# Performance work log

Measured on AMD Instinct MI355X. Metric: run time of the kernel, lower is better.

## Reference

```python
import jax, jax.numpy as jnp
import numpy as np

B, NQ, ISIZE = 8, 2048, 1024
H, D, NA = 8, 128, 8            # num_head, attn_dim, num_anchor
AH = H * D                      # ahsize = 1024
ASZ = NA * D                    # anchor_size = 1024
FH = 4096                       # _fhsize
ISZ_NET = FH * H // NA          # 4096, input dim of self.net
EPS = 1e-6


def setup_inputs() -> dict:
    key = jax.random.key(0)
    ks = jax.random.split(key, 12)
    def u(k, shape, fan_in):
        s = 1.0 / np.sqrt(fan_in)
        return jax.random.uniform(k, shape, jnp.float32, -s, s)
    return {
        "inputs": jax.random.normal(ks[0], (B, NQ, ISIZE), jnp.float32),
        "ln_g": jnp.ones((ISIZE,), jnp.float32),
        "ln_b": jnp.zeros((ISIZE,), jnp.float32),
        "q_anchor": u(ks[1], (H, NA, D), D),
        "W_qkv": u(ks[2], (ISIZE, 3 * AH), ISIZE), "b_qkv": jnp.zeros((3 * AH,), jnp.float32),
        "W_an": u(ks[3], (ASZ, FH), ASZ), "b_an": jnp.zeros((FH,), jnp.float32),
        "W_n1": u(ks[4], (ISZ_NET, AH), ISZ_NET), "b_n1": jnp.zeros((AH,), jnp.float32),
        "W_n2": u(ks[5], (AH, FH), AH), "b_n2": jnp.zeros((FH,), jnp.float32),
        "W_n3": u(ks[6], (FH, AH), FH), "b_n3": jnp.zeros((AH,), jnp.float32),
        "W_k": u(ks[7], (AH, AH), AH), "b_k": jnp.zeros((AH,), jnp.float32),
        "W_o": u(ks[8], (AH, ISIZE), AH), "b_o": jnp.zeros((ISIZE,), jnp.float32),
    }


def reference(inputs, ln_g, ln_b, q_anchor, W_qkv, b_qkv, W_an, b_an,
              W_n1, b_n1, W_n2, b_n2, W_n3, b_n3, W_k, b_k, W_o, b_o):
    b, nq = inputs.shape[:2]
    scale = 1.0 / np.sqrt(D)
    # pre-LayerNorm
    mu = jnp.mean(inputs, -1, keepdims=True)
    var = jnp.mean(jnp.square(inputs - mu), -1, keepdims=True)
    x = (inputs - mu) * jax.lax.rsqrt(var + EPS) * ln_g + ln_b
    # QKV projection
    qkv = (x @ W_qkv + b_qkv).reshape(b, nq, 3, H, D)
    q = jnp.transpose(qkv[:, :, 0], (0, 2, 1, 3))   # [b,H,nq,D]
    k = qkv[:, :, 1]                                  # [b,nq,H,D]
    v = qkv[:, :, 2]                                  # [b,nq,H,D]
    # stage 1: fixed anchors attend over the sequence
    sc1 = jax.nn.softmax(jnp.einsum('had,bnhd->bhan', q_anchor, k) * scale, axis=-1)
    out = jnp.einsum('bhan,bnhd->bhad', sc1, v).reshape(b, H, ASZ)   # [b,H,NA*D]
    # anchor_net (share_head Linear + ReLU)
    out = jax.nn.relu(out @ W_an + b_an)                              # [b,H,FH]
    # regroup head-major -> anchor-major
    out = out.reshape(b, H, NA, FH // NA).transpose(0, 2, 1, 3).reshape(b, NA, ISZ_NET)
    # net: bottleneck Linear -> Linear -> ReLU -> Linear
    out = jax.nn.relu((out @ W_n1 + b_n1) @ W_n2 + b_n2) @ W_n3 + b_n3  # [b,NA,AH]
    # stage 2: queries attend over anchors
    kk = (out @ W_k + b_k).reshape(b, NA, H, D)
    sc2 = jax.nn.softmax(jnp.einsum('bhqd,bahd->bhqa', q, kk) * scale, axis=-1)
    ov = out.reshape(b, NA, H, D)
    y = jnp.einsum('bhqa,bahd->bqhd', sc2, ov).reshape(b, nq, AH)
    return y @ W_o + b_o + inputs
```

## Files before the change

### kernel.cpp

```cpp
#include <hip/hip_runtime.h>
#include <cstdint>
#include <cstddef>

typedef unsigned short u16;
typedef __attribute__((ext_vector_type(8))) short short8;
typedef __attribute__((ext_vector_type(4))) float floatx4;

__device__ __forceinline__ u16 f2bf(float f) {
  unsigned u = __float_as_uint(f);
  u += 0x7fffu + ((u >> 16) & 1u);
  return (u16)(u >> 16);
}
__device__ __forceinline__ float bf2f(u16 s) {
  return __uint_as_float(((unsigned)s) << 16);
}

__global__ __launch_bounds__(256) void ln_kernel(const float* __restrict__ x,
                                                 const float* __restrict__ g,
                                                 const float* __restrict__ bta,
                                                 u16* __restrict__ out) {
  const int row = blockIdx.x;
  const int tid = threadIdx.x;
  const float4 v = ((const float4*)(x + (size_t)row * 1024))[tid];
  float s = v.x + v.y + v.z + v.w;
#pragma unroll
  for (int o = 32; o > 0; o >>= 1) s += __shfl_down(s, o);
  __shared__ float red[4], red2[4];
  const int wv = tid >> 6, ln = tid & 63;
  if (ln == 0) red[wv] = s;
  __syncthreads();
  const float mean = (red[0] + red[1] + red[2] + red[3]) * (1.0f / 1024.0f);
  const float dx = v.x - mean, dy = v.y - mean, dz = v.z - mean, dw = v.w - mean;
  float s2 = dx * dx + dy * dy + dz * dz + dw * dw;
#pragma unroll
  for (int o = 32; o > 0; o >>= 1) s2 += __shfl_down(s2, o);
  if (ln == 0) red2[wv] = s2;
  __syncthreads();
  const float var = (red2[0] + red2[1] + red2[2] + red2[3]) * (1.0f / 1024.0f);
  const float rstd = rsqrtf(var + 1e-6f);
  const float4 gg = ((const float4*)g)[tid];
  const float4 bb = ((const float4*)bta)[tid];
  ushort4 o4;
  o4.x = f2bf(dx * rstd * gg.x + bb.x);
  o4.y = f2bf(dy * rstd * gg.y + bb.y);
  o4.z = f2bf(dz * rstd * gg.z + bb.z);
  o4.w = f2bf(dw * rstd * gg.w + bb.w);
  ((ushort4*)(out + (size_t)row * 1024))[tid] = o4;
}

__global__ __launch_bounds__(256) void transpose_bf16(const float* __restrict__ W,
                                                      u16* __restrict__ WT,
                                                      int K, int N) {
  __shared__ float t[32][33];
  const int kb = blockIdx.x * 32, nb = blockIdx.y * 32;
  const int tx = threadIdx.x & 31, ty = threadIdx.x >> 5;
#pragma unroll
  for (int i = ty; i < 32; i += 8) t[i][tx] = W[(size_t)(kb + i) * N + nb + tx];
  __syncthreads();
#pragma unroll
  for (int i = ty; i < 32; i += 8) WT[(size_t)(nb + i) * K + kb + tx] = f2bf(t[tx][i]);
}


__device__ __forceinline__ void stage2(const u16* __restrict__ src, u16* dst,
                                       int growbase, int kcol, int ld,
                                       int wave, int lane) {
#pragma unroll
  for (int i = 0; i < 2; ++i) {
    const int row = (i * 8 + wave) * 8 + (lane >> 3);
    const u16* gp = src + (size_t)(growbase + row) * ld + kcol + (((lane & 7) ^ (row & 7)) << 3);
    u16* lp = dst + (i * 8 + wave) * 512;
    __builtin_amdgcn_global_load_lds((const __attribute__((address_space(1))) void*)gp,
                                     (__attribute__((address_space(3))) void*)lp, 16, 0, 0);
  }
}

__device__ __forceinline__ void rdA4(short8 (&af)[4][2], const u16* sbuf, int half,
                                     int wr, int fr, int fq) {
#pragma unroll
  for (int mi = 0; mi < 4; ++mi)
#pragma unroll
    for (int ks = 0; ks < 2; ++ks) {
      const int row = half * 128 + wr * 64 + mi * 16 + fr;
      const int kg = ks * 4 + fq;
      af[mi][ks] = *(const short8*)(sbuf + row * 64 + ((kg ^ (row & 7)) << 3));
    }
}

__device__ __forceinline__ void rdB2(short8 (&bfr)[2][2], const u16* sbuf, int half,
                                     int wc, int fr, int fq) {
#pragma unroll
  for (int ni = 0; ni < 2; ++ni)
#pragma unroll
    for (int ks = 0; ks < 2; ++ks) {
      const int row = half * 128 + wc * 32 + ni * 16 + fr;
      const int kg = ks * 4 + fq;
      bfr[ni][ks] = *(const short8*)(sbuf + row * 64 + ((kg ^ (row & 7)) << 3));
    }
}

template <int Q>
__device__ __forceinline__ void mfmaQ(floatx4 (&acc)[4][4][2], const short8 (&af)[4][2],
                                      const short8 (&bfr)[2][2]) {
#pragma unroll
  for (int mi = 0; mi < 4; ++mi)
#pragma unroll
    for (int ni = 0; ni < 2; ++ni)
      acc[Q][mi][ni] = __builtin_amdgcn_mfma_f32_16x16x32_bf16(af[mi][0], bfr[ni][0], acc[Q][mi][ni], 0, 0, 0);
#pragma unroll
  for (int mi = 0; mi < 4; ++mi)
#pragma unroll
    for (int ni = 0; ni < 2; ++ni)
      acc[Q][mi][ni] = __builtin_amdgcn_mfma_f32_16x16x32_bf16(af[mi][1], bfr[ni][1], acc[Q][mi][ni], 0, 0, 0);
}

template <int B_>
__device__ __forceinline__ void gtile(int t, int NT, int K,
                                      u16 (&sA)[2][16384], u16 (&sB)[2][16384],
                                      const u16* __restrict__ A, const u16* __restrict__ BT,
                                      int m0, int n0, int wave, int lane,
                                      int wr, int wc, int fr, int fq,
                                      floatx4 (&acc)[4][4][2]) {
  short8 af[4][2], bfr[2][2];
  rdA4(af, sA[B_], 0, wr, fr, fq);
  rdB2(bfr, sB[B_], 0, wc, fr, fq);
  if (t + 1 < NT) stage2(A, &sA[B_ ^ 1][8192], m0 + 128, (t + 1) << 6, K, wave, lane);
  asm volatile("s_waitcnt lgkmcnt(0)" ::: "memory");
  __builtin_amdgcn_sched_barrier(0);
  __builtin_amdgcn_s_setprio(1);
  mfmaQ<0>(acc, af, bfr);
  __builtin_amdgcn_s_setprio(0);
  rdB2(bfr, sB[B_], 1, wc, fr, fq);
  if (t + 1 < NT) stage2(BT, &sB[B_ ^ 1][0], n0, (t + 1) << 6, K, wave, lane);
  asm volatile("s_waitcnt lgkmcnt(0)" ::: "memory");
  __builtin_amdgcn_sched_barrier(0);
  __builtin_amdgcn_s_setprio(1);
  mfmaQ<1>(acc, af, bfr);
  __builtin_amdgcn_s_setprio(0);
  rdA4(af, sA[B_], 1, wr, fr, fq);
  __builtin_amdgcn_s_barrier();
  if (t + 2 < NT) stage2(A, &sA[B_][0], m0, (t + 2) << 6, K, wave, lane);
  asm volatile("s_waitcnt lgkmcnt(0)" ::: "memory");
  __builtin_amdgcn_sched_barrier(0);
  __builtin_amdgcn_s_setprio(1);
  mfmaQ<2>(acc, af, bfr);
  __builtin_amdgcn_s_setprio(0);
  rdB2(bfr, sB[B_], 0, wc, fr, fq);
  if (t + 2 < NT) stage2(BT, &sB[B_][8192], n0 + 128, (t + 2) << 6, K, wave, lane);
  asm volatile("s_waitcnt lgkmcnt(0)" ::: "memory");
  __builtin_amdgcn_sched_barrier(0);
  __builtin_amdgcn_s_setprio(1);
  mfmaQ<3>(acc, af, bfr);
  __builtin_amdgcn_s_setprio(0);
  if (t + 2 < NT) {
    asm volatile("s_waitcnt vmcnt(4)" ::: "memory");
  } else {
    asm volatile("s_waitcnt vmcnt(0)" ::: "memory");
  }
  __builtin_amdgcn_s_barrier();
}

template <int EPI>
__global__ __launch_bounds__(512, 2) void gemm_bf16(const u16* __restrict__ A,
                                                    const u16* __restrict__ BT,
                                                    const float* __restrict__ bias,
                                                    const float* __restrict__ extra,
                                                    u16* __restrict__ outB,
                                                    float* __restrict__ outF,
                                                    int M, int N, int K) {
  __shared__ u16 sA[2][16384];
  __shared__ u16 sB[2][16384];
  const int tid = threadIdx.x;
  const int wave = tid >> 6, lane = tid & 63;
  const int m0 = blockIdx.x * 256, n0 = blockIdx.y * 256;
  const int wr = wave >> 2, wc = wave & 3;
  const int fr = lane & 15, fq = lane >> 4;
  const int NT = K >> 6;

  floatx4 acc[4][4][2];
  const floatx4 zero = {0.f, 0.f, 0.f, 0.f};
#pragma unroll
  for (int q = 0; q < 4; ++q)
#pragma unroll
    for (int i = 0; i < 4; ++i)
#pragma unroll
      for (int j = 0; j < 2; ++j) acc[q][i][j] = zero;

  stage2(A, &sA[0][0], m0, 0, K, wave, lane);
  stage2(A, &sA[0][8192], m0 + 128, 0, K, wave, lane);
  stage2(BT, &sB[0][0], n0, 0, K, wave, lane);
  stage2(BT, &sB[0][8192], n0 + 128, 0, K, wave, lane);
  stage2(A, &sA[1][0], m0, 64, K, wave, lane);
  stage2(BT, &sB[1][8192], n0 + 128, 64, K, wave, lane);
  asm volatile("s_waitcnt vmcnt(4)" ::: "memory");
  __builtin_amdgcn_s_barrier();

  for (int t = 0; t < NT; t += 2) {
    gtile<0>(t, NT, K, sA, sB, A, BT, m0, n0, wave, lane, wr, wc, fr, fq, acc);
    gtile<1>(t + 1, NT, K, sA, sB, A, BT, m0, n0, wave, lane, wr, wc, fr, fq, acc);
  }

#pragma unroll
  for (int q = 0; q < 4; ++q) {
    const int QM = q >> 1, QN = QM ^ (q & 1);
#pragma unroll
    for (int mi = 0; mi < 4; ++mi)
#pragma unroll
      for (int ni = 0; ni < 2; ++ni)
#pragma unroll
        for (int r = 0; r < 4; ++r) {
          const int m = m0 + QM * 128 + wr * 64 + mi * 16 + fq * 4 + r;
          const int n = n0 + QN * 128 + wc * 32 + ni * 16 + fr;
          const float v = acc[q][mi][ni][r] + bias[n];
          if (EPI == 0)
            outB[(size_t)m * N + n] = f2bf(v);
          else
            outF[(size_t)m * N + n] = v + extra[(size_t)m * N + n];
        }
  }
}

__global__ __launch_bounds__(256) void attn1_scores(const u16* __restrict__ qkv,
                                                    const float* __restrict__ q_anchor,
                                                    float* __restrict__ S) {
  __shared__ float qa[8][128];
  const int tid = threadIdx.x;
  const int chunk = blockIdx.x & 7, bh = blockIdx.x >> 3;
  const int b = bh >> 3, h = bh & 7;
  for (int i = tid; i < 1024; i += 256) qa[i >> 7][i & 127] = q_anchor[h * 1024 + i];
  __syncthreads();
  const float scale = 0.0883883476483184f;
  const int n = chunk * 256 + tid;
  const u16* kp = qkv + (size_t)(b * 2048 + n) * 3072 + 1024 + h * 128;
  float dots[8] = {0, 0, 0, 0, 0, 0, 0, 0};
#pragma unroll 8
  for (int dd = 0; dd < 128; dd += 4) {
    const ushort4 k4 = *(const ushort4*)(kp + dd);
    const float k0 = bf2f(k4.x), k1 = bf2f(k4.y), k2 = bf2f(k4.z), k3 = bf2f(k4.w);
#pragma unroll
    for (int a = 0; a < 8; ++a) {
      const float4 q4 = *(const float4*)&qa[a][dd];
      dots[a] += q4.x * k0 + q4.y * k1 + q4.z * k2 + q4.w * k3;
    }
  }
#pragma unroll
  for (int a = 0; a < 8; ++a) S[((size_t)(bh * 8 + a)) * 2048 + n] = dots[a] * scale;
}

__global__ __launch_bounds__(256) void attn1_softmax(float* __restrict__ S) {
  const int row = blockIdx.x;
  const int tid = threadIdx.x;
  float* Sp = S + (size_t)row * 2048;
  float4 v0 = ((const float4*)Sp)[tid * 2];
  float4 v1 = ((const float4*)Sp)[tid * 2 + 1];
  float mx = fmaxf(fmaxf(fmaxf(v0.x, v0.y), fmaxf(v0.z, v0.w)),
                   fmaxf(fmaxf(v1.x, v1.y), fmaxf(v1.z, v1.w)));
#pragma unroll
  for (int o = 32; o > 0; o >>= 1) mx = fmaxf(mx, __shfl_xor(mx, o));
  __shared__ float red[4];
  const int wv = tid >> 6, ln = tid & 63;
  if (ln == 0) red[wv] = mx;
  __syncthreads();
  mx = fmaxf(fmaxf(red[0], red[1]), fmaxf(red[2], red[3]));
  v0.x = __expf(v0.x - mx); v0.y = __expf(v0.y - mx);
  v0.z = __expf(v0.z - mx); v0.w = __expf(v0.w - mx);
  v1.x = __expf(v1.x - mx); v1.y = __expf(v1.y - mx);
  v1.z = __expf(v1.z - mx); v1.w = __expf(v1.w - mx);
  float sum = v0.x + v0.y + v0.z + v0.w + v1.x + v1.y + v1.z + v1.w;
#pragma unroll
  for (int o = 32; o > 0; o >>= 1) sum += __shfl_xor(sum, o);
  __shared__ float red2[4];
  if (ln == 0) red2[wv] = sum;
  __syncthreads();
  const float inv = 1.f / (red2[0] + red2[1] + red2[2] + red2[3]);
  v0.x *= inv; v0.y *= inv; v0.z *= inv; v0.w *= inv;
  v1.x *= inv; v1.y *= inv; v1.z *= inv; v1.w *= inv;
  ((float4*)Sp)[tid * 2] = v0;
  ((float4*)Sp)[tid * 2 + 1] = v1;
}

__global__ __launch_bounds__(256) void attn1_pv(const u16* __restrict__ qkv,
                                                const float* __restrict__ S,
                                                float* __restrict__ pvpart) {
  __shared__ float P[8][256];
  const int tid = threadIdx.x;
  const int chunk = blockIdx.x & 7, bh = blockIdx.x >> 3;
  const int b = bh >> 3, h = bh & 7;
  for (int i = tid; i < 2048; i += 256) {
    const int a = i >> 8, n = i & 255;
    P[a][n] = S[((size_t)(bh * 8 + a)) * 2048 + chunk * 256 + n];
  }
  __syncthreads();
  const int d = tid & 127, half = tid >> 7;
  const int nbase = chunk * 256 + half * 128;
  const u16* vp = qkv + (size_t)(b * 2048 + nbase) * 3072 + 2048 + h * 128 + d;
  float acc[8] = {0.f};
  for (int n = 0; n < 128; n += 4) {
    const float v0 = bf2f(vp[(size_t)n * 3072]);
    const float v1 = bf2f(vp[(size_t)(n + 1) * 3072]);
    const float v2 = bf2f(vp[(size_t)(n + 2) * 3072]);
    const float v3 = bf2f(vp[(size_t)(n + 3) * 3072]);
#pragma unroll
    for (int a = 0; a < 8; ++a) {
      const float4 s4 = *(const float4*)&P[a][half * 128 + n];
      acc[a] += s4.x * v0 + s4.y * v1 + s4.z * v2 + s4.w * v3;
    }
  }
  const int split = chunk * 2 + half;
#pragma unroll
  for (int a = 0; a < 8; ++a)
    pvpart[((size_t)split * 64 + bh) * 1024 + a * 128 + d] = acc[a];
}

__global__ __launch_bounds__(256) void mlp_mfma(const float* __restrict__ A,
                                                const float* __restrict__ W,
                                                float* __restrict__ part,
                                                int K, int N, int KC) {
  __shared__ float sW[64][33];
  const int tid = threadIdx.x;
  const int lane = tid & 63, wave = tid >> 6;
  const int wm = wave * 16;
  const int n0 = blockIdx.x * 64;
  const int kbeg = blockIdx.y * KC;
  const int l15 = lane & 15, kq8 = (lane >> 4) * 8;
  const int arow = wm + l15;

  floatx4 acc[4];
  const floatx4 zero = {0.f, 0.f, 0.f, 0.f};
#pragma unroll
  for (int j = 0; j < 4; ++j) acc[j] = zero;

  for (int kc = 0; kc < KC; kc += 32) {
    const int kbase = kbeg + kc;
    __syncthreads();
#pragma unroll
    for (int p = 0; p < 8; ++p) {
      const int k = p * 4 + wave;
      sW[lane][k] = W[(size_t)(kbase + k) * N + n0 + lane];
    }
    const float* ap = A + (size_t)arow * K + kbase + kq8;
    const float4 a0 = *(const float4*)ap;
    const float4 a1 = *(const float4*)(ap + 4);
    short8 af;
    af[0] = (short)f2bf(a0.x); af[1] = (short)f2bf(a0.y);
    af[2] = (short)f2bf(a0.z); af[3] = (short)f2bf(a0.w);
    af[4] = (short)f2bf(a1.x); af[5] = (short)f2bf(a1.y);
    af[6] = (short)f2bf(a1.z); af[7] = (short)f2bf(a1.w);
    __syncthreads();
#pragma unroll
    for (int j = 0; j < 4; ++j) {
      const float* wp = &sW[j * 16 + l15][kq8];
      short8 bf;
      bf[0] = (short)f2bf(wp[0]); bf[1] = (short)f2bf(wp[1]);
      bf[2] = (short)f2bf(wp[2]); bf[3] = (short)f2bf(wp[3]);
      bf[4] = (short)f2bf(wp[4]); bf[5] = (short)f2bf(wp[5]);
      bf[6] = (short)f2bf(wp[6]); bf[7] = (short)f2bf(wp[7]);
      acc[j] = __builtin_amdgcn_mfma_f32_16x16x32_bf16(af, bf, acc[j], 0, 0, 0);
    }
  }
  const int q = lane >> 4;
#pragma unroll
  for (int j = 0; j < 4; ++j)
#pragma unroll
    for (int r = 0; r < 4; ++r) {
      const int m = wm + q * 4 + r;
      const int n = n0 + j * 16 + l15;
      part[((size_t)blockIdx.y * 64 + m) * N + n] = acc[j][r];
    }
}

__global__ __launch_bounds__(256) void mlp_reduce(const float* __restrict__ part,
                                                  const float* __restrict__ bias,
                                                  float* __restrict__ out,
                                                  int N, int nsplit, int relu, int perm) {
  const int idx = blockIdx.x * 256 + threadIdx.x;
  const int e = idx * 4;
  if (e >= 64 * N) return;
  const int row = e / N, col = e - row * N;
  float4 acc;
  if (bias) acc = *(const float4*)&bias[col];
  else { acc.x = 0.f; acc.y = 0.f; acc.z = 0.f; acc.w = 0.f; }
  for (int s = 0; s < nsplit; ++s) {
    const float4 p = *(const float4*)&part[((size_t)s * 64 + row) * N + col];
    acc.x += p.x; acc.y += p.y; acc.z += p.z; acc.w += p.w;
  }
  if (relu) {
    acc.x = fmaxf(acc.x, 0.f); acc.y = fmaxf(acc.y, 0.f);
    acc.z = fmaxf(acc.z, 0.f); acc.w = fmaxf(acc.w, 0.f);
  }
  size_t oidx;
  if (!perm) {
    oidx = (size_t)row * N + col;
  } else {
    const int b = row >> 3, h = row & 7;
    oidx = (size_t)(b * 8 + (col >> 9)) * 4096 + h * 512 + (col & 511);
  }
  *(float4*)&out[oidx] = acc;
}

__global__ __launch_bounds__(256) void attn2_kernel(const u16* __restrict__ qkv,
                                                    const float* __restrict__ kk,
                                                    const float* __restrict__ onet,
                                                    u16* __restrict__ y) {
  __shared__ float kkl[8][128];
  __shared__ float ovl[8][128];
  const int tid = threadIdx.x;
  const int chunk = blockIdx.x & 7, bh = blockIdx.x >> 3;
  const int b = bh >> 3, h = bh & 7;
  for (int i = tid; i < 1024; i += 256) {
    const int a = i >> 7, d = i & 127;
    kkl[a][d] = kk[(size_t)(b * 8 + a) * 1024 + h * 128 + d];
    ovl[a][d] = onet[(size_t)(b * 8 + a) * 1024 + h * 128 + d];
  }
  __syncthreads();
  const int n = chunk * 256 + tid;
  const u16* qp = qkv + (size_t)(b * 2048 + n) * 3072 + h * 128;
  float dots[8] = {0, 0, 0, 0, 0, 0, 0, 0};
#pragma unroll 4
  for (int dd = 0; dd < 128; dd += 4) {
    const ushort4 q4 = *(const ushort4*)(qp + dd);
    const float q0 = bf2f(q4.x), q1 = bf2f(q4.y), q2 = bf2f(q4.z), q3 = bf2f(q4.w);
#pragma unroll
    for (int a = 0; a < 8; ++a) {
      const float4 k4 = *(const float4*)&kkl[a][dd];
      dots[a] += k4.x * q0 + k4.y * q1 + k4.z * q2 + k4.w * q3;
    }
  }
  const float scale = 0.0883883476483184f;
  float mx = -1e30f;
#pragma unroll
  for (int a = 0; a < 8; ++a) {
    dots[a] *= scale;
    mx = fmaxf(mx, dots[a]);
  }
  float p[8];
  float sum = 0.f;
#pragma unroll
  for (int a = 0; a < 8; ++a) {
    p[a] = __expf(dots[a] - mx);
    sum += p[a];
  }
  const float inv = 1.f / sum;
#pragma unroll
  for (int a = 0; a < 8; ++a) p[a] *= inv;
  u16* yp = y + (size_t)(b * 2048 + n) * 1024 + h * 128;
#pragma unroll 4
  for (int dd = 0; dd < 128; dd += 4) {
    float a0 = 0, a1 = 0, a2 = 0, a3 = 0;
#pragma unroll
    for (int a = 0; a < 8; ++a) {
      const float4 o4 = *(const float4*)&ovl[a][dd];
      a0 += p[a] * o4.x;
      a1 += p[a] * o4.y;
      a2 += p[a] * o4.z;
      a3 += p[a] * o4.w;
    }
    ushort4 o;
    o.x = f2bf(a0);
    o.y = f2bf(a1);
    o.z = f2bf(a2);
    o.w = f2bf(a3);
    *(ushort4*)(yp + dd) = o;
  }
}

extern "C" void kernel_launch(void* const* d_in, const int* in_sizes, int n_in,
                              void* d_out, int out_size, void* d_ws, size_t ws_size,
                              hipStream_t stream) {
  const float* inputs = (const float*)d_in[0];
  const float* ln_g = (const float*)d_in[1];
  const float* ln_b = (const float*)d_in[2];
  const float* q_anchor = (const float*)d_in[3];
  const float* W_qkv = (const float*)d_in[4];
  const float* b_qkv = (const float*)d_in[5];
  const float* W_an = (const float*)d_in[6];
  const float* b_an = (const float*)d_in[7];
  const float* W_n1 = (const float*)d_in[8];
  const float* b_n1 = (const float*)d_in[9];
  const float* W_n2 = (const float*)d_in[10];
  const float* b_n2 = (const float*)d_in[11];
  const float* W_n3 = (const float*)d_in[12];
  const float* b_n3 = (const float*)d_in[13];
  const float* W_k = (const float*)d_in[14];
  const float* b_k = (const float*)d_in[15];
  const float* W_o = (const float*)d_in[16];
  const float* b_o = (const float*)d_in[17];
  float* out = (float*)d_out;

  char* ws = (char*)d_ws;
  u16* qkv = (u16*)(ws);
  u16* xbf = (u16*)(ws + 100663296);
  float* S = (float*)(ws + 100663296);
  float* part = (float*)(ws + 109051904);
  u16* WqkvT = (u16*)(ws + 134217728);
  u16* WoT = (u16*)(ws + 140509184);
  float* att1 = (float*)(ws + 142606336);
  float* anp = (float*)(ws + 142868480);
  float* h1 = (float*)(ws + 143917056);
  float* h2 = (float*)(ws + 144179200);
  float* onet = (float*)(ws + 145227776);
  float* kkb = (float*)(ws + 145489920);

  ln_kernel<<<16384, 256, 0, stream>>>(inputs, ln_g, ln_b, xbf);
  transpose_bf16<<<dim3(32, 96), 256, 0, stream>>>(W_qkv, WqkvT, 1024, 3072);
  transpose_bf16<<<dim3(32, 32), 256, 0, stream>>>(W_o, WoT, 1024, 1024);
  gemm_bf16<0><<<dim3(64, 12), 512, 0, stream>>>(xbf, WqkvT, b_qkv, nullptr, qkv, nullptr,
                                                 16384, 3072, 1024);
  attn1_scores<<<512, 256, 0, stream>>>(qkv, q_anchor, S);
  attn1_softmax<<<512, 256, 0, stream>>>(S);
  attn1_pv<<<512, 256, 0, stream>>>(qkv, S, part);
  mlp_reduce<<<64, 256, 0, stream>>>(part, nullptr, att1, 1024, 16, 0, 0);
  mlp_mfma<<<dim3(64, 8), 256, 0, stream>>>(att1, W_an, part, 1024, 4096, 128);
  mlp_reduce<<<256, 256, 0, stream>>>(part, b_an, anp, 4096, 8, 1, 1);
  mlp_mfma<<<dim3(16, 32), 256, 0, stream>>>(anp, W_n1, part, 4096, 1024, 128);
  mlp_reduce<<<64, 256, 0, stream>>>(part, b_n1, h1, 1024, 32, 0, 0);
  mlp_mfma<<<dim3(64, 8), 256, 0, stream>>>(h1, W_n2, part, 1024, 4096, 128);
  mlp_reduce<<<256, 256, 0, stream>>>(part, b_n2, h2, 4096, 8, 1, 0);
  mlp_mfma<<<dim3(16, 32), 256, 0, stream>>>(h2, W_n3, part, 4096, 1024, 128);
  mlp_reduce<<<64, 256, 0, stream>>>(part, b_n3, onet, 1024, 32, 0, 0);
  mlp_mfma<<<dim3(16, 16), 256, 0, stream>>>(onet, W_k, part, 1024, 1024, 64);
  mlp_reduce<<<64, 256, 0, stream>>>(part, b_k, kkb, 1024, 16, 0, 0);
  attn2_kernel<<<512, 256, 0, stream>>>(qkv, kkb, onet, xbf);
  gemm_bf16<1><<<dim3(64, 4), 512, 0, stream>>>(xbf, WoT, b_o, inputs, nullptr, out,
                                                16384, 1024, 1024);
}
```

Before: 586.4 us.

## Switch GEMM to 32x32x16 MFMA with precomputed LDS offsets and reordered staging

Replaces the 16x16x32 bf16 MFMA tiling in the main GEMM with 32x32x16 instructions (2x1 fragments per quarter, 4 k-steps). LDS read offsets and global staging pointers are precomputed once per thread instead of recomputed each tile, and the quarter schedule reuses B fragments across quarters with a partial lgkmcnt wait. The intent is to cut LDS read traffic and issue overhead per FLOP. It also reshapes the epilogue to the 32x32 output layout, which keeps scattered per-element stores.

```diff
diff --git a/kernel.cpp b/kernel.cpp
--- a/kernel.cpp
+++ b/kernel.cpp
@@ -5,6 +5,7 @@
 typedef unsigned short u16;
 typedef __attribute__((ext_vector_type(8))) short short8;
 typedef __attribute__((ext_vector_type(4))) float floatx4;
+typedef __attribute__((ext_vector_type(16))) float floatx16;
 
 __device__ __forceinline__ u16 f2bf(float f) {
   unsigned u = __float_as_uint(f);
@@ -62,95 +63,75 @@
 }
 
 
-__device__ __forceinline__ void stage2(const u16* __restrict__ src, u16* dst,
-                                       int growbase, int kcol, int ld,
-                                       int wave, int lane) {
-#pragma unroll
-  for (int i = 0; i < 2; ++i) {
-    const int row = (i * 8 + wave) * 8 + (lane >> 3);
-    const u16* gp = src + (size_t)(growbase + row) * ld + kcol + (((lane & 7) ^ (row & 7)) << 3);
-    u16* lp = dst + (i * 8 + wave) * 512;
-    __builtin_amdgcn_global_load_lds((const __attribute__((address_space(1))) void*)gp,
-                                     (__attribute__((address_space(3))) void*)lp, 16, 0, 0);
-  }
-}
-
-__device__ __forceinline__ void rdA4(short8 (&af)[4][2], const u16* sbuf, int half,
-                                     int wr, int fr, int fq) {
-#pragma unroll
-  for (int mi = 0; mi < 4; ++mi)
-#pragma unroll
-    for (int ks = 0; ks < 2; ++ks) {
-      const int row = half * 128 + wr * 64 + mi * 16 + fr;
-      const int kg = ks * 4 + fq;
-      af[mi][ks] = *(const short8*)(sbuf + row * 64 + ((kg ^ (row & 7)) << 3));
-    }
-}
-
-__device__ __forceinline__ void rdB2(short8 (&bfr)[2][2], const u16* sbuf, int half,
-                                     int wc, int fr, int fq) {
-#pragma unroll
-  for (int ni = 0; ni < 2; ++ni)
-#pragma unroll
-    for (int ks = 0; ks < 2; ++ks) {
-      const int row = half * 128 + wc * 32 + ni * 16 + fr;
-      const int kg = ks * 4 + fq;
-      bfr[ni][ks] = *(const short8*)(sbuf + row * 64 + ((kg ^ (row & 7)) << 3));
-    }
+__device__ __forceinline__ void stageG(const u16* __restrict__ gp, u16* lp, int K) {
+  __builtin_amdgcn_global_load_lds((const __attribute__((address_space(1))) void*)gp,
+                                   (__attribute__((address_space(3))) void*)lp, 16, 0, 0);
+  __builtin_amdgcn_global_load_lds((const __attribute__((address_space(1))) void*)(gp + ((size_t)K << 6)),
+                                   (__attribute__((address_space(3))) void*)(lp + 4096), 16, 0, 0);
+}
+
+__device__ __forceinline__ void rdA(short8 (&af)[2][4], const u16* sbuf, const int (&ab)[4],
+                                    int halfoff) {
+#pragma unroll
+  for (int mi = 0; mi < 2; ++mi)
+#pragma unroll
+    for (int ks = 0; ks < 4; ++ks)
+      af[mi][ks] = *(const short8*)(sbuf + halfoff + mi * 2048 + ab[ks]);
+}
+__device__ __forceinline__ void rdB(short8 (&bf)[4], const u16* sbuf, const int (&bb)[4],
+                                    int halfoff) {
+#pragma unroll
+  for (int ks = 0; ks < 4; ++ks)
+    bf[ks] = *(const short8*)(sbuf + halfoff + bb[ks]);
 }
 
 template <int Q>
-__device__ __forceinline__ void mfmaQ(floatx4 (&acc)[4][4][2], const short8 (&af)[4][2],
-                                      const short8 (&bfr)[2][2]) {
-#pragma unroll
-  for (int mi = 0; mi < 4; ++mi)
-#pragma unroll
-    for (int ni = 0; ni < 2; ++ni)
-      acc[Q][mi][ni] = __builtin_amdgcn_mfma_f32_16x16x32_bf16(af[mi][0], bfr[ni][0], acc[Q][mi][ni], 0, 0, 0);
-#pragma unroll
-  for (int mi = 0; mi < 4; ++mi)
-#pragma unroll
-    for (int ni = 0; ni < 2; ++ni)
-      acc[Q][mi][ni] = __builtin_amdgcn_mfma_f32_16x16x32_bf16(af[mi][1], bfr[ni][1], acc[Q][mi][ni], 0, 0, 0);
+__device__ __forceinline__ void mfmaQ(floatx16 (&acc)[4][2], const short8 (&af)[2][4],
+                                      const short8 (&bf)[4]) {
+#pragma unroll
+  for (int ks = 0; ks < 4; ++ks)
+#pragma unroll
+    for (int mi = 0; mi < 2; ++mi)
+      acc[Q][mi] = __builtin_amdgcn_mfma_f32_32x32x16_bf16(af[mi][ks], bf[ks], acc[Q][mi], 0, 0, 0);
 }
 
 template <int B_>
 __device__ __forceinline__ void gtile(int t, int NT, int K,
                                       u16 (&sA)[2][16384], u16 (&sB)[2][16384],
-                                      const u16* __restrict__ A, const u16* __restrict__ BT,
-                                      int m0, int n0, int wave, int lane,
-                                      int wr, int wc, int fr, int fq,
-                                      floatx4 (&acc)[4][4][2]) {
-  short8 af[4][2], bfr[2][2];
-  rdA4(af, sA[B_], 0, wr, fr, fq);
-  rdB2(bfr, sB[B_], 0, wc, fr, fq);
-  if (t + 1 < NT) stage2(A, &sA[B_ ^ 1][8192], m0 + 128, (t + 1) << 6, K, wave, lane);
+                                      const u16* gA_lo, const u16* gA_hi,
+                                      const u16* gB_lo, const u16* gB_hi,
+                                      u16* ldsA_cur, u16* ldsA_alt,
+                                      u16* ldsB_cur, u16* ldsB_alt,
+                                      const int (&ab)[4], const int (&bb)[4],
+                                      floatx16 (&acc)[4][2]) {
+  short8 af[2][4], bf0[4], bf1[4];
+  rdA(af, sA[B_], ab, 0);
+  rdB(bf0, sB[B_], bb, 0);
+  __builtin_amdgcn_sched_barrier(0);
+  if (t + 1 < NT) stageG(gA_hi + ((t + 1) << 6), ldsA_alt + 8192, K);
+  rdB(bf1, sB[B_], bb, 8192);
+  asm volatile("s_waitcnt lgkmcnt(4)" ::: "memory");
+  __builtin_amdgcn_sched_barrier(0);
+  __builtin_amdgcn_s_setprio(1);
+  mfmaQ<0>(acc, af, bf0);
+  __builtin_amdgcn_s_setprio(0);
+  if (t + 1 < NT) stageG(gB_lo + ((t + 1) << 6), ldsB_alt, K);
   asm volatile("s_waitcnt lgkmcnt(0)" ::: "memory");
   __builtin_amdgcn_sched_barrier(0);
   __builtin_amdgcn_s_setprio(1);
-  mfmaQ<0>(acc, af, bfr);
+  mfmaQ<1>(acc, af, bf1);
   __builtin_amdgcn_s_setprio(0);
-  rdB2(bfr, sB[B_], 1, wc, fr, fq);
-  if (t + 1 < NT) stage2(BT, &sB[B_ ^ 1][0], n0, (t + 1) << 6, K, wave, lane);
+  rdA(af, sA[B_], ab, 8192);
+  __builtin_amdgcn_s_barrier();
+  if (t + 2 < NT) stageG(gA_lo + ((t + 2) << 6), ldsA_cur, K);
   asm volatile("s_waitcnt lgkmcnt(0)" ::: "memory");
   __builtin_amdgcn_sched_barrier(0);
   __builtin_amdgcn_s_setprio(1);
-  mfmaQ<1>(acc, af, bfr);
+  mfmaQ<2>(acc, af, bf1);
   __builtin_amdgcn_s_setprio(0);
-  rdA4(af, sA[B_], 1, wr, fr, fq);
-  __builtin_amdgcn_s_barrier();
-  if (t + 2 < NT) stage2(A, &sA[B_][0], m0, (t + 2) << 6, K, wave, lane);
-  asm volatile("s_waitcnt lgkmcnt(0)" ::: "memory");
-  __builtin_amdgcn_sched_barrier(0);
+  if (t + 2 < NT) stageG(gB_hi + ((t + 2) << 6), ldsB_cur + 8192, K);
   __builtin_amdgcn_s_setprio(1);
-  mfmaQ<2>(acc, af, bfr);
-  __builtin_amdgcn_s_setprio(0);
-  rdB2(bfr, sB[B_], 0, wc, fr, fq);
-  if (t + 2 < NT) stage2(BT, &sB[B_][8192], n0 + 128, (t + 2) << 6, K, wave, lane);
-  asm volatile("s_waitcnt lgkmcnt(0)" ::: "memory");
-  __builtin_amdgcn_sched_barrier(0);
-  __builtin_amdgcn_s_setprio(1);
-  mfmaQ<3>(acc, af, bfr);
+  mfmaQ<3>(acc, af, bf0);
   __builtin_amdgcn_s_setprio(0);
   if (t + 2 < NT) {
     asm volatile("s_waitcnt vmcnt(4)" ::: "memory");
@@ -174,49 +155,67 @@
   const int wave = tid >> 6, lane = tid & 63;
   const int m0 = blockIdx.x * 256, n0 = blockIdx.y * 256;
   const int wr = wave >> 2, wc = wave & 3;
-  const int fr = lane & 15, fq = lane >> 4;
+  const int l31 = lane & 31, l5 = lane >> 5, l7 = lane & 7;
   const int NT = K >> 6;
 
-  floatx4 acc[4][4][2];
-  const floatx4 zero = {0.f, 0.f, 0.f, 0.f};
+  int ab[4], bb[4];
+#pragma unroll
+  for (int ks = 0; ks < 4; ++ks) {
+    const int xr = ((((ks << 1) + l5) ^ l7) << 3);
+    ab[ks] = (wr * 64 + l31) * 64 + xr;
+    bb[ks] = (wc * 32 + l31) * 64 + xr;
+  }
+  const int srow = wave * 8 + (lane >> 3);
+  const int scol = ((lane & 7) ^ (srow & 7)) << 3;
+  const u16* gA_lo = A + (size_t)(m0 + srow) * K + scol;
+  const u16* gA_hi = A + (size_t)(m0 + 128 + srow) * K + scol;
+  const u16* gB_lo = BT + (size_t)(n0 + srow) * K + scol;
+  const u16* gB_hi = BT + (size_t)(n0 + 128 + srow) * K + scol;
+
+  floatx16 acc[4][2];
 #pragma unroll
   for (int q = 0; q < 4; ++q)
 #pragma unroll
-    for (int i = 0; i < 4; ++i)
-#pragma unroll
-      for (int j = 0; j < 2; ++j) acc[q][i][j] = zero;
-
-  stage2(A, &sA[0][0], m0, 0, K, wave, lane);
-  stage2(A, &sA[0][8192], m0 + 128, 0, K, wave, lane);
-  stage2(BT, &sB[0][0], n0, 0, K, wave, lane);
-  stage2(BT, &sB[0][8192], n0 + 128, 0, K, wave, lane);
-  stage2(A, &sA[1][0], m0, 64, K, wave, lane);
-  stage2(BT, &sB[1][8192], n0 + 128, 64, K, wave, lane);
+    for (int mi = 0; mi < 2; ++mi)
+#pragma unroll
+      for (int r = 0; r < 16; ++r) acc[q][mi][r] = 0.f;
+
+  stageG(gA_lo, &sA[0][0] + wave * 512, K);
+  stageG(gA_hi, &sA[0][8192] + wave * 512, K);
+  stageG(gB_lo, &sB[0][0] + wave * 512, K);
+  stageG(gB_hi, &sB[0][8192] + wave * 512, K);
+  stageG(gA_lo + 64, &sA[1][0] + wave * 512, K);
+  stageG(gB_hi + 64, &sB[1][8192] + wave * 512, K);
   asm volatile("s_waitcnt vmcnt(4)" ::: "memory");
   __builtin_amdgcn_s_barrier();
 
   for (int t = 0; t < NT; t += 2) {
-    gtile<0>(t, NT, K, sA, sB, A, BT, m0, n0, wave, lane, wr, wc, fr, fq, acc);
-    gtile<1>(t + 1, NT, K, sA, sB, A, BT, m0, n0, wave, lane, wr, wc, fr, fq, acc);
+    gtile<0>(t, NT, K, sA, sB, gA_lo, gA_hi, gB_lo, gB_hi,
+             &sA[0][0] + wave * 512, &sA[1][0] + wave * 512,
+             &sB[0][0] + wave * 512, &sB[1][0] + wave * 512, ab, bb, acc);
+    gtile<1>(t + 1, NT, K, sA, sB, gA_lo, gA_hi, gB_lo, gB_hi,
+             &sA[1][0] + wave * 512, &sA[0][0] + wave * 512,
+             &sB[1][0] + wave * 512, &sB[0][0] + wave * 512, ab, bb, acc);
   }
 
 #pragma unroll
   for (int q = 0; q < 4; ++q) {
     const int QM = q >> 1, QN = QM ^ (q & 1);
-#pragma unroll
-    for (int mi = 0; mi < 4; ++mi)
-#pragma unroll
-      for (int ni = 0; ni < 2; ++ni)
-#pragma unroll
-        for (int r = 0; r < 4; ++r) {
-          const int m = m0 + QM * 128 + wr * 64 + mi * 16 + fq * 4 + r;
-          const int n = n0 + QN * 128 + wc * 32 + ni * 16 + fr;
-          const float v = acc[q][mi][ni][r] + bias[n];
-          if (EPI == 0)
-            outB[(size_t)m * N + n] = f2bf(v);
-          else
-            outF[(size_t)m * N + n] = v + extra[(size_t)m * N + n];
-        }
+    const int n = n0 + QN * 128 + wc * 32 + l31;
+    const float bs = bias[n];
+#pragma unroll
+    for (int mi = 0; mi < 2; ++mi) {
+      const int mb = m0 + QM * 128 + wr * 64 + mi * 32 + 4 * l5;
+#pragma unroll
+      for (int reg = 0; reg < 16; ++reg) {
+        const int m = mb + (reg & 3) + 8 * (reg >> 2);
+        const float v = acc[q][mi][reg] + bs;
+        if (EPI == 0)
+          outB[(size_t)m * N + n] = f2bf(v);
+        else
+          outF[(size_t)m * N + n] = v + extra[(size_t)m * N + n];
+      }
+    }
   }
 }
 
```

After: 601.3 us. +2.5%, slower.
